# Optimization experiments

Hardware: AMD Instinct MI355X
Metric: run time of the kernel (lower is better)

The kernel has to match this reference:

```python
import jax, jax.numpy as jnp
import numpy as np

N, IN_F, OUT_F = 4096, 4096, 4096
THRESH = 0.05


def setup_inputs() -> dict:
    key = jax.random.key(0)
    k_x, k_w = jax.random.split(key)
    last_out = jax.random.normal(k_x, (N, IN_F), dtype=jnp.float32)
    # learned weight buffer, [out_features, in_features] like torch Linear
    weight = jax.random.normal(k_w, (OUT_F, IN_F), dtype=jnp.float32) * (1.0 / np.sqrt(IN_F))
    threshold = jnp.float32(THRESH)
    return {"last_out": last_out, "weight": weight, "threshold": threshold}


def reference(last_out, weight, threshold):
    # rtp_linear: runtime threshold pruning — activations with |x| <= threshold
    # are skipped (treated as zero) in the matmul. Bias buffer is unused
    # (dead code in the original forward).
    x = jnp.where(jnp.abs(last_out) > threshold, last_out, 0.0)
    # y[n, o] = sum_i x[n, i] * W[o, i]
    return jnp.einsum("ni,oi->no", x, weight)
```

## Files before the change

### kernel.cpp

```cpp
#include <hip/hip_runtime.h>
#include <hip/hip_bf16.h>

#define M_DIM 4096
#define N_DIM 4096
#define K_DIM 4096

typedef __attribute__((ext_vector_type(8))) __bf16 bf16x8;
typedef __attribute__((ext_vector_type(8))) short short8;
typedef __attribute__((ext_vector_type(8))) unsigned short ushort8;
typedef __attribute__((ext_vector_type(4))) float f32x4;

__device__ __forceinline__ void gload_lds16(const void* g, void* l) {
    __builtin_amdgcn_global_load_lds(
        (const __attribute__((address_space(1))) void*)g,
        (__attribute__((address_space(3))) void*)l,
        16, 0, 0);
}

__device__ __forceinline__ bf16x8 ld8(const unsigned short* p) {
    short8 r = *reinterpret_cast<const short8*>(p);
    return __builtin_bit_cast(bf16x8, r);
}

__global__ void prune_cvt(const float* __restrict__ in,
                          unsigned short* __restrict__ out,
                          const float* __restrict__ thrp, int n8) {
    const float thr = thrp ? thrp[0] : -1.0f;
    const int stride = gridDim.x * blockDim.x;
    for (int idx = blockIdx.x * blockDim.x + threadIdx.x; idx < n8; idx += stride) {
        const float4* p = reinterpret_cast<const float4*>(in) + 2 * (size_t)idx;
        float4 v0 = p[0];
        float4 v1 = p[1];
        float v[8] = {v0.x, v0.y, v0.z, v0.w, v1.x, v1.y, v1.z, v1.w};
        ushort8 o;
#pragma unroll
        for (int j = 0; j < 8; ++j) {
            float f = v[j];
            f = (fabsf(f) > thr) ? f : 0.0f;
            __hip_bfloat16 hh = __float2bfloat16(f);
            o[j] = *reinterpret_cast<unsigned short*>(&hh);
        }
        *reinterpret_cast<ushort8*>(out + 8 * (size_t)idx) = o;
    }
}

__global__ __launch_bounds__(512, 2) void gemm_8phase(
        const unsigned short* __restrict__ A,
        const unsigned short* __restrict__ B,
        float* __restrict__ C) {
    __shared__ __align__(16) unsigned short lds[65536];

    const int tid  = threadIdx.x;
    const int lane = tid & 63;
    const int wid  = tid >> 6;
    const int wr   = wid >> 2;
    const int wc   = wid & 3;

    const int bid = blockIdx.x;
    const int swz = (bid & 7) * 32 + (bid >> 3);
    const int bm = (swz >> 4) * 256;
    const int bn = (swz & 15) * 256;

    const int g  = tid & 255;
    const int ah = tid >> 8;
    const int arow = bm + ah * 128 + (g >> 3);
    const int acol = 8 * ((g & 7) ^ ((g >> 3) & 7));
    const unsigned short* Asrc = A + (size_t)arow * K_DIM + acol;
    const int AdstE = ah * 8192 + g * 8;

    const int h = lane + 64 * wr;
    const int brow = bn + wc * 64 + (h >> 3);
    const int bcol = 8 * ((h & 7) ^ ((h >> 3) & 7));
    const unsigned short* Bsrc = B + (size_t)brow * K_DIM + bcol;
    const int BdstE = wc * 4096 + h * 8;

#define SA(dstb, j, kg) gload_lds16(Asrc + (size_t)(32*(j))*K_DIM + (kg), (dstb) + AdstE + 2048*(j))
#define SB(dstb, j, kg) gload_lds16(Bsrc + (size_t)(16*(j))*K_DIM + (kg), (dstb) + BdstE + 1024*(j))

    const int fr  = lane & 15;
    const int kq4 = lane >> 4;
    const int rowOffA = (wr * 128 + fr) * 64;
    const int rowOffB = (wc * 64 + fr) * 64;
    const int sk0 = 8 * ((kq4    ) ^ (fr & 7));
    const int sk1 = 8 * ((kq4 + 4) ^ (fr & 7));

    f32x4 acc[8][4] = {};

#define MFMA16(q, A00, A10, A01, A11)                                                              \
    __builtin_amdgcn_s_setprio(1);                                                                 \
    _Pragma("unroll")                                                                              \
    for (int n = 0; n < 4; ++n) {                                                                  \
        acc[2*(q)][n]   = __builtin_amdgcn_mfma_f32_16x16x32_bf16(A00, bfr[n][0], acc[2*(q)][n], 0, 0, 0);   \
        acc[2*(q)+1][n] = __builtin_amdgcn_mfma_f32_16x16x32_bf16(A10, bfr[n][0], acc[2*(q)+1][n], 0, 0, 0); \
        acc[2*(q)][n]   = __builtin_amdgcn_mfma_f32_16x16x32_bf16(A01, bfr[n][1], acc[2*(q)][n], 0, 0, 0);   \
        acc[2*(q)+1][n] = __builtin_amdgcn_mfma_f32_16x16x32_bf16(A11, bfr[n][1], acc[2*(q)+1][n], 0, 0, 0); \
    }                                                                                              \
    __builtin_amdgcn_s_setprio(0);

    SB(lds + 32768, 0, 0); SB(lds + 32768, 1, 0); SB(lds + 32768, 2, 0); SB(lds + 32768, 3, 0);
    SA(lds,         0, 0); SA(lds,         1, 0); SA(lds,         2, 0); SA(lds,         3, 0);
    asm volatile("s_waitcnt vmcnt(3)" ::: "memory");
    asm volatile("s_barrier" ::: "memory");

    for (int t = 0; t < 64; ++t) {
        const int cur = t & 1, nxt = cur ^ 1;
        const unsigned short* Ab = lds + cur * 16384;
        const unsigned short* Bb = lds + 32768 + cur * 16384;
        unsigned short* AbN = lds + nxt * 16384;
        unsigned short* BbN = lds + 32768 + nxt * 16384;
        const int kn = (t < 63 ? (t + 1) : 63) * 64;

        bf16x8 bfr[4][2];
        {
#pragma unroll
            for (int n = 0; n < 4; ++n) {
                bfr[n][0] = ld8(Bb + rowOffB + n * 1024 + sk0);
                bfr[n][1] = ld8(Bb + rowOffB + n * 1024 + sk1);
            }
            bf16x8 a00 = ld8(Ab + rowOffA + 0 * 1024 + sk0);
            bf16x8 a10 = ld8(Ab + rowOffA + 1 * 1024 + sk0);
            bf16x8 a01 = ld8(Ab + rowOffA + 0 * 1024 + sk1);
            bf16x8 a11 = ld8(Ab + rowOffA + 1 * 1024 + sk1);
            SB(BbN, 0, kn); SB(BbN, 1, kn); SB(BbN, 2, kn); SB(BbN, 3, kn);
            asm volatile("s_barrier" ::: "memory");
            MFMA16(0, a00, a10, a01, a11);
            asm volatile("s_waitcnt vmcnt(6)" ::: "memory");
            asm volatile("s_barrier" ::: "memory");
        }
        {
            bf16x8 a00 = ld8(Ab + rowOffA + 2 * 1024 + sk0);
            bf16x8 a10 = ld8(Ab + rowOffA + 3 * 1024 + sk0);
            bf16x8 a01 = ld8(Ab + rowOffA + 2 * 1024 + sk1);
            bf16x8 a11 = ld8(Ab + rowOffA + 3 * 1024 + sk1);
            SA(AbN, 0, kn); SA(AbN, 1, kn);
            asm volatile("s_barrier" ::: "memory");
            MFMA16(1, a00, a10, a01, a11);
            asm volatile("s_waitcnt vmcnt(7)" ::: "memory");
            asm volatile("s_barrier" ::: "memory");
        }
        {
            bf16x8 a00 = ld8(Ab + rowOffA + 4 * 1024 + sk0);
            bf16x8 a10 = ld8(Ab + rowOffA + 5 * 1024 + sk0);
            bf16x8 a01 = ld8(Ab + rowOffA + 4 * 1024 + sk1);
            bf16x8 a11 = ld8(Ab + rowOffA + 5 * 1024 + sk1);
            SA(AbN, 2, kn); SA(AbN, 3, kn);
            asm volatile("s_barrier" ::: "memory");
            MFMA16(2, a00, a10, a01, a11);
            asm volatile("s_waitcnt vmcnt(8)" ::: "memory");
            asm volatile("s_barrier" ::: "memory");
        }
        {
            bf16x8 a00 = ld8(Ab + rowOffA + 6 * 1024 + sk0);
            bf16x8 a10 = ld8(Ab + rowOffA + 7 * 1024 + sk0);
            bf16x8 a01 = ld8(Ab + rowOffA + 6 * 1024 + sk1);
            bf16x8 a11 = ld8(Ab + rowOffA + 7 * 1024 + sk1);
            asm volatile("s_barrier" ::: "memory");
            MFMA16(3, a00, a10, a01, a11);
            asm volatile("s_waitcnt vmcnt(3)" ::: "memory");
            asm volatile("s_barrier" ::: "memory");
        }
    }

    asm volatile("s_waitcnt vmcnt(0)" ::: "memory");

    const int crow = bm + wr * 128 + kq4 * 4;
    const int ccol = bn + wc * 64 + fr;
#pragma unroll
    for (int m = 0; m < 8; ++m)
#pragma unroll
        for (int n = 0; n < 4; ++n)
#pragma unroll
            for (int j = 0; j < 4; ++j)
                C[(size_t)(crow + m * 16 + j) * N_DIM + ccol + n * 16] = acc[m][n][j];
}

__global__ void gemm_f32_fallback(const float* __restrict__ A,
                                  const float* __restrict__ B,
                                  float* __restrict__ C,
                                  const float* __restrict__ thrp) {
    __shared__ float As[32][33];
    __shared__ float Bs[32][33];
    const float thr = thrp[0];
    const int tx = threadIdx.x, ty = threadIdx.y;
    const int row = blockIdx.y * 32 + ty;
    float acc = 0.0f;
    for (int k0 = 0; k0 < K_DIM; k0 += 32) {
        float a = A[(size_t)row * K_DIM + k0 + tx];
        As[ty][tx] = (fabsf(a) > thr) ? a : 0.0f;
        Bs[ty][tx] = B[(size_t)(blockIdx.x * 32 + ty) * K_DIM + k0 + tx];
        __syncthreads();
#pragma unroll 8
        for (int kk = 0; kk < 32; ++kk)
            acc += As[ty][kk] * Bs[tx][kk];
        __syncthreads();
    }
    C[(size_t)row * N_DIM + blockIdx.x * 32 + tx] = acc;
}

extern "C" void kernel_launch(void* const* d_in, const int* in_sizes, int n_in,
                              void* d_out, int out_size, void* d_ws, size_t ws_size,
                              hipStream_t stream) {
    const float* x    = (const float*)d_in[0];
    const float* w    = (const float*)d_in[1];
    const float* thrp = (const float*)d_in[2];
    float* out = (float*)d_out;

    const size_t elems = (size_t)M_DIM * K_DIM;
    if (ws_size >= 2 * elems * sizeof(unsigned short)) {
        unsigned short* Ab = (unsigned short*)d_ws;
        unsigned short* Bb = Ab + elems;
        const int n8 = (int)(elems / 8);
        prune_cvt<<<2048, 256, 0, stream>>>(x, Ab, thrp, n8);
        prune_cvt<<<2048, 256, 0, stream>>>(w, Bb, nullptr, n8);
        gemm_8phase<<<dim3(256), dim3(512), 0, stream>>>(Ab, Bb, out);
    } else {
        dim3 grid(N_DIM / 32, M_DIM / 32), blk(32, 32);
        gemm_f32_fallback<<<grid, blk, 0, stream>>>(x, w, out, thrp);
    }
}
```

Before: 150.7 us.

## Software-pipeline A fragment LDS reads across phases and fuse prune kernels

Restructures the GEMM main loop so each phase issues LDS reads for the next A fragment before running the current MFMA block, and preloads the first fragment of the next k-tile at the end of the iteration. Barriers and vmcnt waits are reshuffled to fit this schedule, and the MFMA issue order is split into two passes over n. The two prune/convert launches are merged into one kernel to save a launch. This hides LDS latency behind MFMA work, at the cost of more live registers and tighter wait counts that must still be correct.

```diff
diff --git a/kernel.cpp b/kernel.cpp
--- a/kernel.cpp
+++ b/kernel.cpp
@@ -22,25 +22,33 @@
     return __builtin_bit_cast(bf16x8, r);
 }
 
-__global__ void prune_cvt(const float* __restrict__ in,
-                          unsigned short* __restrict__ out,
-                          const float* __restrict__ thrp, int n8) {
-    const float thr = thrp ? thrp[0] : -1.0f;
+__global__ void prune_cvt2(const float* __restrict__ x,
+                           const float* __restrict__ w,
+                           unsigned short* __restrict__ xb,
+                           unsigned short* __restrict__ wb,
+                           const float* __restrict__ thrp, int n8) {
+    const float thr = thrp[0];
     const int stride = gridDim.x * blockDim.x;
-    for (int idx = blockIdx.x * blockDim.x + threadIdx.x; idx < n8; idx += stride) {
-        const float4* p = reinterpret_cast<const float4*>(in) + 2 * (size_t)idx;
+    const int total = 2 * n8;
+    for (int idx = blockIdx.x * blockDim.x + threadIdx.x; idx < total; idx += stride) {
+        const bool isx = idx < n8;
+        const int j = isx ? idx : idx - n8;
+        const float* src = isx ? x : w;
+        unsigned short* dst = isx ? xb : wb;
+        const float te = isx ? thr : -1.0f;
+        const float4* p = reinterpret_cast<const float4*>(src) + 2 * (size_t)j;
         float4 v0 = p[0];
         float4 v1 = p[1];
         float v[8] = {v0.x, v0.y, v0.z, v0.w, v1.x, v1.y, v1.z, v1.w};
         ushort8 o;
 #pragma unroll
-        for (int j = 0; j < 8; ++j) {
-            float f = v[j];
-            f = (fabsf(f) > thr) ? f : 0.0f;
+        for (int e = 0; e < 8; ++e) {
+            float f = v[e];
+            f = (fabsf(f) > te) ? f : 0.0f;
             __hip_bfloat16 hh = __float2bfloat16(f);
-            o[j] = *reinterpret_cast<unsigned short*>(&hh);
+            o[e] = *reinterpret_cast<unsigned short*>(&hh);
         }
-        *reinterpret_cast<ushort8*>(out + 8 * (size_t)idx) = o;
+        *reinterpret_cast<ushort8*>(dst + 8 * (size_t)j) = o;
     }
 }
 
@@ -86,12 +94,16 @@
 
     f32x4 acc[8][4] = {};
 
+    bf16x8 bfr[4][2];
 #define MFMA16(q, A00, A10, A01, A11)                                                              \
     __builtin_amdgcn_s_setprio(1);                                                                 \
     _Pragma("unroll")                                                                              \
     for (int n = 0; n < 4; ++n) {                                                                  \
         acc[2*(q)][n]   = __builtin_amdgcn_mfma_f32_16x16x32_bf16(A00, bfr[n][0], acc[2*(q)][n], 0, 0, 0);   \
         acc[2*(q)+1][n] = __builtin_amdgcn_mfma_f32_16x16x32_bf16(A10, bfr[n][0], acc[2*(q)+1][n], 0, 0, 0); \
+    }                                                                                              \
+    _Pragma("unroll")                                                                              \
+    for (int n = 0; n < 4; ++n) {                                                                  \
         acc[2*(q)][n]   = __builtin_amdgcn_mfma_f32_16x16x32_bf16(A01, bfr[n][1], acc[2*(q)][n], 0, 0, 0);   \
         acc[2*(q)+1][n] = __builtin_amdgcn_mfma_f32_16x16x32_bf16(A11, bfr[n][1], acc[2*(q)+1][n], 0, 0, 0); \
     }                                                                                              \
@@ -99,64 +111,62 @@
 
     SB(lds + 32768, 0, 0); SB(lds + 32768, 1, 0); SB(lds + 32768, 2, 0); SB(lds + 32768, 3, 0);
     SA(lds,         0, 0); SA(lds,         1, 0); SA(lds,         2, 0); SA(lds,         3, 0);
-    asm volatile("s_waitcnt vmcnt(3)" ::: "memory");
+    asm volatile("s_waitcnt vmcnt(2)" ::: "memory");
     asm volatile("s_barrier" ::: "memory");
+
+    bf16x8 p00 = ld8(lds + rowOffA + 0 * 1024 + sk0);
+    bf16x8 p10 = ld8(lds + rowOffA + 1 * 1024 + sk0);
+    bf16x8 p01 = ld8(lds + rowOffA + 0 * 1024 + sk1);
+    bf16x8 p11 = ld8(lds + rowOffA + 1 * 1024 + sk1);
 
     for (int t = 0; t < 64; ++t) {
         const int cur = t & 1, nxt = cur ^ 1;
-        const unsigned short* Ab = lds + cur * 16384;
-        const unsigned short* Bb = lds + 32768 + cur * 16384;
+        const unsigned short* Ab  = lds + cur * 16384;
+        const unsigned short* Bb  = lds + 32768 + cur * 16384;
         unsigned short* AbN = lds + nxt * 16384;
         unsigned short* BbN = lds + 32768 + nxt * 16384;
-        const int kn = (t < 63 ? (t + 1) : 63) * 64;
-
-        bf16x8 bfr[4][2];
+        const unsigned short* AbNr = AbN;
+        const int kn = (t < 63 ? t + 1 : 63) * 64;
+
         {
 #pragma unroll
             for (int n = 0; n < 4; ++n) {
                 bfr[n][0] = ld8(Bb + rowOffB + n * 1024 + sk0);
                 bfr[n][1] = ld8(Bb + rowOffB + n * 1024 + sk1);
             }
-            bf16x8 a00 = ld8(Ab + rowOffA + 0 * 1024 + sk0);
-            bf16x8 a10 = ld8(Ab + rowOffA + 1 * 1024 + sk0);
-            bf16x8 a01 = ld8(Ab + rowOffA + 0 * 1024 + sk1);
-            bf16x8 a11 = ld8(Ab + rowOffA + 1 * 1024 + sk1);
+            bf16x8 q00 = ld8(Ab + rowOffA + 2 * 1024 + sk0);
+            bf16x8 q10 = ld8(Ab + rowOffA + 3 * 1024 + sk0);
+            bf16x8 q01 = ld8(Ab + rowOffA + 2 * 1024 + sk1);
+            bf16x8 q11 = ld8(Ab + rowOffA + 3 * 1024 + sk1);
             SB(BbN, 0, kn); SB(BbN, 1, kn); SB(BbN, 2, kn); SB(BbN, 3, kn);
-            asm volatile("s_barrier" ::: "memory");
-            MFMA16(0, a00, a10, a01, a11);
+            MFMA16(0, p00, p10, p01, p11);
+            asm volatile("s_waitcnt vmcnt(5)" ::: "memory");
+            asm volatile("s_barrier" ::: "memory");
+
+            bf16x8 r00 = ld8(Ab + rowOffA + 4 * 1024 + sk0);
+            bf16x8 r10 = ld8(Ab + rowOffA + 5 * 1024 + sk0);
+            bf16x8 r01 = ld8(Ab + rowOffA + 4 * 1024 + sk1);
+            bf16x8 r11 = ld8(Ab + rowOffA + 5 * 1024 + sk1);
+            SA(AbN, 0, kn); SA(AbN, 1, kn);
+            MFMA16(1, q00, q10, q01, q11);
             asm volatile("s_waitcnt vmcnt(6)" ::: "memory");
             asm volatile("s_barrier" ::: "memory");
-        }
-        {
-            bf16x8 a00 = ld8(Ab + rowOffA + 2 * 1024 + sk0);
-            bf16x8 a10 = ld8(Ab + rowOffA + 3 * 1024 + sk0);
-            bf16x8 a01 = ld8(Ab + rowOffA + 2 * 1024 + sk1);
-            bf16x8 a11 = ld8(Ab + rowOffA + 3 * 1024 + sk1);
-            SA(AbN, 0, kn); SA(AbN, 1, kn);
-            asm volatile("s_barrier" ::: "memory");
-            MFMA16(1, a00, a10, a01, a11);
-            asm volatile("s_waitcnt vmcnt(7)" ::: "memory");
-            asm volatile("s_barrier" ::: "memory");
-        }
-        {
-            bf16x8 a00 = ld8(Ab + rowOffA + 4 * 1024 + sk0);
-            bf16x8 a10 = ld8(Ab + rowOffA + 5 * 1024 + sk0);
-            bf16x8 a01 = ld8(Ab + rowOffA + 4 * 1024 + sk1);
-            bf16x8 a11 = ld8(Ab + rowOffA + 5 * 1024 + sk1);
+
+            bf16x8 s00 = ld8(Ab + rowOffA + 6 * 1024 + sk0);
+            bf16x8 s10 = ld8(Ab + rowOffA + 7 * 1024 + sk0);
+            bf16x8 s01 = ld8(Ab + rowOffA + 6 * 1024 + sk1);
+            bf16x8 s11 = ld8(Ab + rowOffA + 7 * 1024 + sk1);
             SA(AbN, 2, kn); SA(AbN, 3, kn);
-            asm volatile("s_barrier" ::: "memory");
-            MFMA16(2, a00, a10, a01, a11);
-            asm volatile("s_waitcnt vmcnt(8)" ::: "memory");
-            asm volatile("s_barrier" ::: "memory");
-        }
-        {
-            bf16x8 a00 = ld8(Ab + rowOffA + 6 * 1024 + sk0);
-            bf16x8 a10 = ld8(Ab + rowOffA + 7 * 1024 + sk0);
-            bf16x8 a01 = ld8(Ab + rowOffA + 6 * 1024 + sk1);
-            bf16x8 a11 = ld8(Ab + rowOffA + 7 * 1024 + sk1);
-            asm volatile("s_barrier" ::: "memory");
-            MFMA16(3, a00, a10, a01, a11);
+            MFMA16(2, r00, r10, r01, r11);
             asm volatile("s_waitcnt vmcnt(3)" ::: "memory");
+            asm volatile("s_barrier" ::: "memory");
+
+            p00 = ld8(AbNr + rowOffA + 0 * 1024 + sk0);
+            p10 = ld8(AbNr + rowOffA + 1 * 1024 + sk0);
+            p01 = ld8(AbNr + rowOffA + 0 * 1024 + sk1);
+            p11 = ld8(AbNr + rowOffA + 1 * 1024 + sk1);
+            MFMA16(3, s00, s10, s01, s11);
+            asm volatile("s_waitcnt vmcnt(2)" ::: "memory");
             asm volatile("s_barrier" ::: "memory");
         }
     }
@@ -210,8 +220,7 @@
         unsigned short* Ab = (unsigned short*)d_ws;
         unsigned short* Bb = Ab + elems;
         const int n8 = (int)(elems / 8);
-        prune_cvt<<<2048, 256, 0, stream>>>(x, Ab, thrp, n8);
-        prune_cvt<<<2048, 256, 0, stream>>>(w, Bb, nullptr, n8);
+        prune_cvt2<<<2048, 256, 0, stream>>>(x, w, Ab, Bb, thrp, n8);
         gemm_8phase<<<dim3(256), dim3(512), 0, stream>>>(Ab, Bb, out);
     } else {
         dim3 grid(N_DIM / 32, M_DIM / 32), blk(32, 32);
```

Result: faster. 146.4 us (-2.8%).
